# Kernel tuning notes

Measured on AMD Instinct MI355X. Metric: run time of the kernel, lower is better.

Reference implementation:

```python
import jax, jax.numpy as jnp
import numpy as np

SIGMA2 = 1.9 * 1.9   # LJ sigma^2 (Angstrom^2)
EPS = 0.2            # LJ well depth
R2_SOFT = 0.25       # softening to keep energies finite for random dofs


def _local_ht(dofs):
    """dofs [..., 9] -> local homogeneous transform [..., 4, 4].
    Uses (phi, theta, d) bond-style dofs: R = Rz(phi) @ Ry(theta),
    translation d along the rotated x-axis."""
    phi, theta = dofs[..., 0], dofs[..., 1]
    d = 1.5 + 0.25 * jnp.tanh(dofs[..., 2])  # bond length ~1.25..1.75 A
    cp, sp = jnp.cos(phi), jnp.sin(phi)
    ct, st = jnp.cos(theta), jnp.sin(theta)
    r00, r01, r02 = cp * ct, -sp, cp * st
    r10, r11, r12 = sp * ct, cp, sp * st
    r20, r21, r22 = -st, jnp.zeros_like(ct), ct
    tx, ty, tz = d * r00, d * r10, d * r20
    zero, one = jnp.zeros_like(phi), jnp.ones_like(phi)
    ht = jnp.stack([
        jnp.stack([r00, r01, r02, tx], -1),
        jnp.stack([r10, r11, r12, ty], -1),
        jnp.stack([r20, r21, r22, tz], -1),
        jnp.stack([zero, zero, zero, one], -1),
    ], -2)
    return ht


def _forward_kin(full_dofs, P, A):
    # per-pose chain kinforest: cumulative left-product of local HTs
    ht = _local_ht(full_dofs.reshape(P, A, 9))  # [P, A, 4, 4]
    compose = lambda a, b: jnp.einsum('...ij,...jk->...ik', a, b)
    cum = jax.lax.associative_scan(compose, ht, axis=1)
    return cum[..., :3, 3].reshape(-1, 3)  # [P*A, 3]


def _lj_score(coords):
    # coords [P, A, 3] -> per-pose softened LJ energy [P]
    sq = jnp.sum(coords * coords, axis=-1)                 # [P, A]
    G = jnp.einsum('pad,pbd->pab', coords, coords)         # [P, A, A] GEMM
    r2 = sq[:, :, None] + sq[:, None, :] - 2.0 * G + R2_SOFT
    inv6 = (SIGMA2 / r2) ** 3
    e = 4.0 * EPS * (inv6 * inv6 - inv6)
    A = coords.shape[1]
    mask = jnp.triu(jnp.ones((A, A), dtype=coords.dtype), k=1)  # i < j
    return jnp.sum(e * mask, axis=(1, 2))


def setup_inputs() -> dict:
    key = jax.random.key(0)
    k1, k2 = jax.random.split(key)
    P, A = 4, 4096
    full_dofs = 0.5 * jax.random.normal(k1, (P * A, 9), dtype=jnp.float32)
    pose_stack_coords = 5.0 * jax.random.normal(k2, (P, A, 3), dtype=jnp.float32)
    kinforest_id = jnp.arange(P * A, dtype=jnp.int64)
    return {"full_dofs": full_dofs, "pose_stack_coords": pose_stack_coords,
            "kinforest_id": kinforest_id}


def reference(full_dofs, pose_stack_coords, kinforest_id):
    P, A, _ = pose_stack_coords.shape
    kincoords = _forward_kin(full_dofs, P, A)  # [P*A, 3]
    coords = pose_stack_coords.reshape(-1, 3).at[kinforest_id].set(kincoords)
    coords = coords.reshape(P, A, 3)
    return _lj_score(coords)  # [P]
```

## Files before the change

kernel.cpp:

```cpp
#include <hip/hip_runtime.h>
#include <math.h>

#define A_ATOMS 4096
#define P_POSES 4
#define N_TOT   (A_ATOMS * P_POSES)
#define TILE    128
#define NTILES  (A_ATOMS / TILE)
#define NPAIRT  (NTILES * (NTILES + 1) / 2)

#define SEG     64
#define NSEG    (A_ATOMS / SEG)
#define APPLY_T 256
#define APPLY_B (A_ATOMS / APPLY_T)

typedef float v2f __attribute__((ext_vector_type(2)));

__device__ __constant__ float c_SIGMA2  = 1.9f * 1.9f;
__device__ __constant__ float c_4EPS    = 0.8f;
__device__ __constant__ float c_R2SOFT  = 0.25f;

struct RT { float m[12]; };

__device__ inline RT rt_identity() {
    RT v;
    v.m[0]=1.f; v.m[1]=0.f; v.m[2]=0.f;  v.m[3]=0.f;
    v.m[4]=0.f; v.m[5]=1.f; v.m[6]=0.f;  v.m[7]=0.f;
    v.m[8]=0.f; v.m[9]=0.f; v.m[10]=1.f; v.m[11]=0.f;
    return v;
}

__device__ inline RT rt_compose(const RT& a, const RT& b) {
    RT c;
#pragma unroll
    for (int i = 0; i < 3; ++i) {
        float a0 = a.m[i*4+0], a1 = a.m[i*4+1], a2 = a.m[i*4+2];
        c.m[i*4+0] = fmaf(a0, b.m[0], fmaf(a1, b.m[4],  a2*b.m[8]));
        c.m[i*4+1] = fmaf(a0, b.m[1], fmaf(a1, b.m[5],  a2*b.m[9]));
        c.m[i*4+2] = fmaf(a0, b.m[2], fmaf(a1, b.m[6],  a2*b.m[10]));
        c.m[i*4+3] = fmaf(a0, b.m[3], fmaf(a1, b.m[7],  fmaf(a2, b.m[11], a.m[i*4+3])));
    }
    return c;
}

__device__ inline RT rt_shfl_up(const RT& a, int off) {
    RT r;
#pragma unroll
    for (int i = 0; i < 12; ++i) r.m[i] = __shfl_up(a.m[i], off, 64);
    return r;
}

__device__ inline RT local_ht(const float* __restrict__ dof) {
    float phi = dof[0], th = dof[1];
    float d = fmaf(0.25f, tanhf(dof[2]), 1.5f);
    float sp, cp, st, ct;
    sincosf(phi, &sp, &cp);
    sincosf(th,  &st, &ct);
    RT h;
    h.m[0] = cp*ct; h.m[1] = -sp; h.m[2]  = cp*st; h.m[3]  = d*cp*ct;
    h.m[4] = sp*ct; h.m[5] =  cp; h.m[6]  = sp*st; h.m[7]  = d*sp*ct;
    h.m[8] = -st;   h.m[9] = 0.f; h.m[10] = ct;    h.m[11] = -d*st;
    return h;
}

__global__ __launch_bounds__(SEG) void fk_scan(const float* __restrict__ dofs,
                                               float* __restrict__ Tx,
                                               float* __restrict__ Ty,
                                               float* __restrict__ Tz,
                                               float4* __restrict__ S0,
                                               float4* __restrict__ S1,
                                               float4* __restrict__ S2) {
    const int pose = blockIdx.x >> 6;
    const int seg  = blockIdx.x & (NSEG - 1);
    const int lane = threadIdx.x;
    const int g    = pose * A_ATOMS + seg * SEG + lane;

    RT v = local_ht(dofs + (size_t)g * 9);

#pragma unroll
    for (int off = 1; off < 64; off <<= 1) {
        RT l = rt_shfl_up(v, off);
        if (lane >= off) v = rt_compose(l, v);
    }

    Tx[g] = v.m[3]; Ty[g] = v.m[7]; Tz[g] = v.m[11];

    if (lane == 63) {
        int s = pose * NSEG + seg;
        S0[s] = make_float4(v.m[0], v.m[1], v.m[2],  v.m[3]);
        S1[s] = make_float4(v.m[4], v.m[5], v.m[6],  v.m[7]);
        S2[s] = make_float4(v.m[8], v.m[9], v.m[10], v.m[11]);
    }
}

__global__ __launch_bounds__(APPLY_T) void fk_apply(const int* __restrict__ kid,
                                                    const float* __restrict__ Tx,
                                                    const float* __restrict__ Ty,
                                                    const float* __restrict__ Tz,
                                                    const float4* __restrict__ S0,
                                                    const float4* __restrict__ S1,
                                                    const float4* __restrict__ S2,
                                                    float* __restrict__ X,
                                                    float* __restrict__ Y,
                                                    float* __restrict__ Z,
                                                    float* __restrict__ out) {
    __shared__ float4 e0[NSEG], e1[NSEG], e2[NSEG];

    const int pose = blockIdx.y;
    const int blk  = blockIdx.x;
    const int tid  = threadIdx.x;
    if (blk == 0 && tid == 0) out[pose] = 0.f;

    if (tid < 64) {
        int s = pose * NSEG + tid;
        float4 a0 = S0[s], a1 = S1[s], a2 = S2[s];
        RT v;
        v.m[0]=a0.x; v.m[1]=a0.y; v.m[2]=a0.z;  v.m[3]=a0.w;
        v.m[4]=a1.x; v.m[5]=a1.y; v.m[6]=a1.z;  v.m[7]=a1.w;
        v.m[8]=a2.x; v.m[9]=a2.y; v.m[10]=a2.z; v.m[11]=a2.w;
#pragma unroll
        for (int off = 1; off < 64; off <<= 1) {
            RT l = rt_shfl_up(v, off);
            if (tid >= off) v = rt_compose(l, v);
        }
        RT ex = rt_shfl_up(v, 1);
        if (tid == 0) ex = rt_identity();
        e0[tid] = make_float4(ex.m[0], ex.m[1], ex.m[2],  ex.m[3]);
        e1[tid] = make_float4(ex.m[4], ex.m[5], ex.m[6],  ex.m[7]);
        e2[tid] = make_float4(ex.m[8], ex.m[9], ex.m[10], ex.m[11]);
    }
    __syncthreads();

    const int a = blk * APPLY_T + tid;
    const int g = pose * A_ATOMS + a;
    float rx = Tx[g], ry = Ty[g], rz = Tz[g];
    float4 x0 = e0[a >> 6], x1 = e1[a >> 6], x2 = e2[a >> 6];
    float tx = fmaf(x0.x, rx, fmaf(x0.y, ry, fmaf(x0.z, rz, x0.w)));
    float ty = fmaf(x1.x, rx, fmaf(x1.y, ry, fmaf(x1.z, rz, x1.w)));
    float tz = fmaf(x2.x, rx, fmaf(x2.y, ry, fmaf(x2.z, rz, x2.w)));
    int dst = kid[g];
    X[dst] = tx; Y[dst] = ty; Z[dst] = tz;
}

__global__ __launch_bounds__(256) void lj_kernel(const float* __restrict__ X,
                                                 const float* __restrict__ Y,
                                                 const float* __restrict__ Z,
                                                 float* __restrict__ out) {
    const int pose = blockIdx.y;
    int rr = blockIdx.x, bi = 0;
    while (rr >= NTILES - bi) { rr -= NTILES - bi; ++bi; }
    const int bj = bi + rr;

    __shared__ float sxi[TILE], syi[TILE], szi[TILE];
    __shared__ float sxj[TILE], syj[TILE], szj[TILE];

    const int tid = threadIdx.x;
    const float* Xp = X + pose * A_ATOMS;
    const float* Yp = Y + pose * A_ATOMS;
    const float* Zp = Z + pose * A_ATOMS;

    if (tid < TILE) {
        int gi = bi * TILE + tid;
        sxi[tid] = Xp[gi]; syi[tid] = Yp[gi]; szi[tid] = Zp[gi];
    } else {
        int t = tid - TILE;
        int gj = bj * TILE + t;
        sxj[t] = Xp[gj]; syj[t] = Yp[gj]; szj[t] = Zp[gj];
    }
    __syncthreads();

    const int i0 = (tid & 15) * 8;
    const int j0 = (tid >> 4) * 8;

    const float SIG2 = c_SIGMA2, SOFT = c_R2SOFT;
    float acc = 0.f;

    if (bi != bj) {
        float xi[8], yi[8], zi[8];
#pragma unroll
        for (int k = 0; k < 8; ++k) {
            xi[k] = sxi[i0 + k]; yi[k] = syi[i0 + k]; zi[k] = szi[i0 + k];
        }
        v2f xj2[4], yj2[4], zj2[4];
#pragma unroll
        for (int p = 0; p < 4; ++p) {
            xj2[p] = (v2f){sxj[j0 + 2*p], sxj[j0 + 2*p + 1]};
            yj2[p] = (v2f){syj[j0 + 2*p], syj[j0 + 2*p + 1]};
            zj2[p] = (v2f){szj[j0 + 2*p], szj[j0 + 2*p + 1]};
        }
        const v2f soft2 = (v2f){SOFT, SOFT};
        v2f acc2 = (v2f){0.f, 0.f};
#pragma unroll
        for (int p = 0; p < 4; ++p) {
#pragma unroll
            for (int k = 0; k < 8; ++k) {
                v2f dx = xi[k] - xj2[p];
                v2f dy = yi[k] - yj2[p];
                v2f dz = zi[k] - zj2[p];
                v2f r2 = __builtin_elementwise_fma(dx, dx,
                         __builtin_elementwise_fma(dy, dy,
                         __builtin_elementwise_fma(dz, dz, soft2)));
                v2f rc = (v2f){__builtin_amdgcn_rcpf(r2.x), __builtin_amdgcn_rcpf(r2.y)};
                v2f t  = SIG2 * rc;
                v2f i6 = t * t * t;
                acc2 += __builtin_elementwise_fma(i6, i6, -i6);
            }
        }
        acc = acc2.x + acc2.y;
    } else {
        float xi[8], yi[8], zi[8], xj[8], yj[8], zj[8];
#pragma unroll
        for (int k = 0; k < 8; ++k) {
            xi[k] = sxi[i0 + k]; yi[k] = syi[i0 + k]; zi[k] = szi[i0 + k];
            xj[k] = sxj[j0 + k]; yj[k] = syj[j0 + k]; zj[k] = szj[j0 + k];
        }
#pragma unroll
        for (int jj = 0; jj < 8; ++jj) {
            int j = j0 + jj;
#pragma unroll
            for (int k = 0; k < 8; ++k) {
                float dx = xi[k] - xj[jj], dy = yi[k] - yj[jj], dz = zi[k] - zj[jj];
                float r2 = fmaf(dx, dx, fmaf(dy, dy, fmaf(dz, dz, SOFT)));
                float t  = SIG2 * __builtin_amdgcn_rcpf(r2);
                float i6 = t * t * t;
                float hh = fmaf(i6, i6, -i6);
                acc += ((i0 + k) < j) ? hh : 0.f;
            }
        }
    }
    acc *= c_4EPS;

#pragma unroll
    for (int off = 32; off > 0; off >>= 1) acc += __shfl_down(acc, off, 64);

    __shared__ float wsum[4];
    int lane = tid & 63, wid = tid >> 6;
    if (lane == 0) wsum[wid] = acc;
    __syncthreads();
    if (tid == 0) {
        float s = wsum[0] + wsum[1] + wsum[2] + wsum[3];
        atomicAdd(out + pose, s);
    }
}

extern "C" void kernel_launch(void* const* d_in, const int* in_sizes, int n_in,
                              void* d_out, int out_size, void* d_ws, size_t ws_size,
                              hipStream_t stream) {
    (void)in_sizes; (void)n_in; (void)out_size; (void)ws_size;
    const float* dofs = (const float*)d_in[0];
    const int*   kid  = (const int*)d_in[2];
    float*       out  = (float*)d_out;

    float* X  = (float*)d_ws;
    float* Y  = X + N_TOT;
    float* Z  = Y + N_TOT;
    float* Tx = Z + N_TOT;
    float* Ty = Tx + N_TOT;
    float* Tz = Ty + N_TOT;
    float4* S0 = (float4*)(Tz + N_TOT);
    float4* S1 = S0 + P_POSES * NSEG;
    float4* S2 = S1 + P_POSES * NSEG;

    fk_scan<<<P_POSES * NSEG, SEG, 0, stream>>>(dofs, Tx, Ty, Tz, S0, S1, S2);
    dim3 agrid(APPLY_B, P_POSES);
    fk_apply<<<agrid, APPLY_T, 0, stream>>>(kid, Tx, Ty, Tz, S0, S1, S2, X, Y, Z, out);
    dim3 grid(NPAIRT, P_POSES);
    lj_kernel<<<grid, 256, 0, stream>>>(X, Y, Z, out);
}
```

Baseline: 90.91 us.

## Fold segment-prefix apply into LJ tile load, shrink fk_apply to tiny prefix kernel

Result: slower. 93.25 us (+2.6%).

```diff
diff --git a/kernel.cpp b/kernel.cpp
--- a/kernel.cpp
+++ b/kernel.cpp
@@ -10,8 +10,7 @@
 
 #define SEG     64
 #define NSEG    (A_ATOMS / SEG)
-#define APPLY_T 256
-#define APPLY_B (A_ATOMS / APPLY_T)
+#define NSEG_TOT (P_POSES * NSEG)
 
 typedef float v2f __attribute__((ext_vector_type(2)));
 
@@ -63,9 +62,8 @@
 }
 
 __global__ __launch_bounds__(SEG) void fk_scan(const float* __restrict__ dofs,
-                                               float* __restrict__ Tx,
-                                               float* __restrict__ Ty,
-                                               float* __restrict__ Tz,
+                                               const int* __restrict__ kid,
+                                               float4* __restrict__ TS,
                                                float4* __restrict__ S0,
                                                float4* __restrict__ S1,
                                                float4* __restrict__ S2) {
@@ -82,68 +80,49 @@
         if (lane >= off) v = rt_compose(l, v);
     }
 
-    Tx[g] = v.m[3]; Ty[g] = v.m[7]; Tz[g] = v.m[11];
+    const int wseg = pose * NSEG + seg;
+    TS[kid[g]] = make_float4(v.m[3], v.m[7], v.m[11], __int_as_float(wseg));
 
     if (lane == 63) {
-        int s = pose * NSEG + seg;
-        S0[s] = make_float4(v.m[0], v.m[1], v.m[2],  v.m[3]);
-        S1[s] = make_float4(v.m[4], v.m[5], v.m[6],  v.m[7]);
-        S2[s] = make_float4(v.m[8], v.m[9], v.m[10], v.m[11]);
-    }
-}
-
-__global__ __launch_bounds__(APPLY_T) void fk_apply(const int* __restrict__ kid,
-                                                    const float* __restrict__ Tx,
-                                                    const float* __restrict__ Ty,
-                                                    const float* __restrict__ Tz,
-                                                    const float4* __restrict__ S0,
-                                                    const float4* __restrict__ S1,
-                                                    const float4* __restrict__ S2,
-                                                    float* __restrict__ X,
-                                                    float* __restrict__ Y,
-                                                    float* __restrict__ Z,
-                                                    float* __restrict__ out) {
-    __shared__ float4 e0[NSEG], e1[NSEG], e2[NSEG];
-
-    const int pose = blockIdx.y;
-    const int blk  = blockIdx.x;
-    const int tid  = threadIdx.x;
-    if (blk == 0 && tid == 0) out[pose] = 0.f;
-
-    if (tid < 64) {
-        int s = pose * NSEG + tid;
-        float4 a0 = S0[s], a1 = S1[s], a2 = S2[s];
-        RT v;
-        v.m[0]=a0.x; v.m[1]=a0.y; v.m[2]=a0.z;  v.m[3]=a0.w;
-        v.m[4]=a1.x; v.m[5]=a1.y; v.m[6]=a1.z;  v.m[7]=a1.w;
-        v.m[8]=a2.x; v.m[9]=a2.y; v.m[10]=a2.z; v.m[11]=a2.w;
-#pragma unroll
-        for (int off = 1; off < 64; off <<= 1) {
-            RT l = rt_shfl_up(v, off);
-            if (tid >= off) v = rt_compose(l, v);
-        }
-        RT ex = rt_shfl_up(v, 1);
-        if (tid == 0) ex = rt_identity();
-        e0[tid] = make_float4(ex.m[0], ex.m[1], ex.m[2],  ex.m[3]);
-        e1[tid] = make_float4(ex.m[4], ex.m[5], ex.m[6],  ex.m[7]);
-        e2[tid] = make_float4(ex.m[8], ex.m[9], ex.m[10], ex.m[11]);
-    }
-    __syncthreads();
-
-    const int a = blk * APPLY_T + tid;
-    const int g = pose * A_ATOMS + a;
-    float rx = Tx[g], ry = Ty[g], rz = Tz[g];
-    float4 x0 = e0[a >> 6], x1 = e1[a >> 6], x2 = e2[a >> 6];
-    float tx = fmaf(x0.x, rx, fmaf(x0.y, ry, fmaf(x0.z, rz, x0.w)));
-    float ty = fmaf(x1.x, rx, fmaf(x1.y, ry, fmaf(x1.z, rz, x1.w)));
-    float tz = fmaf(x2.x, rx, fmaf(x2.y, ry, fmaf(x2.z, rz, x2.w)));
-    int dst = kid[g];
-    X[dst] = tx; Y[dst] = ty; Z[dst] = tz;
-}
-
-__global__ __launch_bounds__(256) void lj_kernel(const float* __restrict__ X,
-                                                 const float* __restrict__ Y,
-                                                 const float* __restrict__ Z,
+        S0[wseg] = make_float4(v.m[0], v.m[1], v.m[2],  v.m[3]);
+        S1[wseg] = make_float4(v.m[4], v.m[5], v.m[6],  v.m[7]);
+        S2[wseg] = make_float4(v.m[8], v.m[9], v.m[10], v.m[11]);
+    }
+}
+
+__global__ __launch_bounds__(SEG) void fk_eprefix(const float4* __restrict__ S0,
+                                                  const float4* __restrict__ S1,
+                                                  const float4* __restrict__ S2,
+                                                  float4* __restrict__ E0,
+                                                  float4* __restrict__ E1,
+                                                  float4* __restrict__ E2,
+                                                  float* __restrict__ out) {
+    const int pose = blockIdx.x;
+    const int lane = threadIdx.x;
+    if (lane == 0) out[pose] = 0.f;
+
+    const int s = pose * NSEG + lane;
+    float4 a0 = S0[s], a1 = S1[s], a2 = S2[s];
+    RT v;
+    v.m[0]=a0.x; v.m[1]=a0.y; v.m[2]=a0.z;  v.m[3]=a0.w;
+    v.m[4]=a1.x; v.m[5]=a1.y; v.m[6]=a1.z;  v.m[7]=a1.w;
+    v.m[8]=a2.x; v.m[9]=a2.y; v.m[10]=a2.z; v.m[11]=a2.w;
+#pragma unroll
+    for (int off = 1; off < 64; off <<= 1) {
+        RT l = rt_shfl_up(v, off);
+        if (lane >= off) v = rt_compose(l, v);
+    }
+    RT ex = rt_shfl_up(v, 1);
+    if (lane == 0) ex = rt_identity();
+    E0[s] = make_float4(ex.m[0], ex.m[1], ex.m[2],  ex.m[3]);
+    E1[s] = make_float4(ex.m[4], ex.m[5], ex.m[6],  ex.m[7]);
+    E2[s] = make_float4(ex.m[8], ex.m[9], ex.m[10], ex.m[11]);
+}
+
+__global__ __launch_bounds__(256) void lj_kernel(const float4* __restrict__ TS,
+                                                 const float4* __restrict__ E0,
+                                                 const float4* __restrict__ E1,
+                                                 const float4* __restrict__ E2,
                                                  float* __restrict__ out) {
     const int pose = blockIdx.y;
     int rr = blockIdx.x, bi = 0;
@@ -154,17 +133,16 @@
     __shared__ float sxj[TILE], syj[TILE], szj[TILE];
 
     const int tid = threadIdx.x;
-    const float* Xp = X + pose * A_ATOMS;
-    const float* Yp = Y + pose * A_ATOMS;
-    const float* Zp = Z + pose * A_ATOMS;
-
-    if (tid < TILE) {
-        int gi = bi * TILE + tid;
-        sxi[tid] = Xp[gi]; syi[tid] = Yp[gi]; szi[tid] = Zp[gi];
-    } else {
-        int t = tid - TILE;
-        int gj = bj * TILE + t;
-        sxj[t] = Xp[gj]; syj[t] = Yp[gj]; szj[t] = Zp[gj];
+    {
+        const int a_loc = (tid < TILE) ? (bi * TILE + tid) : (bj * TILE + (tid - TILE));
+        float4 t4 = TS[pose * A_ATOMS + a_loc];
+        const int wseg = __float_as_int(t4.w);
+        float4 x0 = E0[wseg], x1 = E1[wseg], x2 = E2[wseg];
+        float x = fmaf(x0.x, t4.x, fmaf(x0.y, t4.y, fmaf(x0.z, t4.z, x0.w)));
+        float y = fmaf(x1.x, t4.x, fmaf(x1.y, t4.y, fmaf(x1.z, t4.z, x1.w)));
+        float z = fmaf(x2.x, t4.x, fmaf(x2.y, t4.y, fmaf(x2.z, t4.z, x2.w)));
+        if (tid < TILE) { sxi[tid] = x; syi[tid] = y; szi[tid] = z; }
+        else            { sxj[tid - TILE] = x; syj[tid - TILE] = y; szj[tid - TILE] = z; }
     }
     __syncthreads();
 
@@ -250,19 +228,16 @@
     const int*   kid  = (const int*)d_in[2];
     float*       out  = (float*)d_out;
 
-    float* X  = (float*)d_ws;
-    float* Y  = X + N_TOT;
-    float* Z  = Y + N_TOT;
-    float* Tx = Z + N_TOT;
-    float* Ty = Tx + N_TOT;
-    float* Tz = Ty + N_TOT;
-    float4* S0 = (float4*)(Tz + N_TOT);
-    float4* S1 = S0 + P_POSES * NSEG;
-    float4* S2 = S1 + P_POSES * NSEG;
-
-    fk_scan<<<P_POSES * NSEG, SEG, 0, stream>>>(dofs, Tx, Ty, Tz, S0, S1, S2);
-    dim3 agrid(APPLY_B, P_POSES);
-    fk_apply<<<agrid, APPLY_T, 0, stream>>>(kid, Tx, Ty, Tz, S0, S1, S2, X, Y, Z, out);
+    float4* TS = (float4*)d_ws;
+    float4* S0 = TS + N_TOT;
+    float4* S1 = S0 + NSEG_TOT;
+    float4* S2 = S1 + NSEG_TOT;
+    float4* E0 = S2 + NSEG_TOT;
+    float4* E1 = E0 + NSEG_TOT;
+    float4* E2 = E1 + NSEG_TOT;
+
+    fk_scan<<<NSEG_TOT, SEG, 0, stream>>>(dofs, kid, TS, S0, S1, S2);
+    fk_eprefix<<<P_POSES, SEG, 0, stream>>>(S0, S1, S2, E0, E1, E2, out);
     dim3 grid(NPAIRT, P_POSES);
-    lj_kernel<<<grid, 256, 0, stream>>>(X, Y, Z, out);
-}
+    lj_kernel<<<grid, 256, 0, stream>>>(TS, E0, E1, E2, out);
+}
```

## Process strips of four j-tiles per block with register-prefetched next tile

Applied to the files above, without the earlier changes.

Result: faster. 76.84 us (-15.5%).

```diff
diff --git a/kernel.cpp b/kernel.cpp
--- a/kernel.cpp
+++ b/kernel.cpp
@@ -6,7 +6,9 @@
 #define N_TOT   (A_ATOMS * P_POSES)
 #define TILE    128
 #define NTILES  (A_ATOMS / TILE)
-#define NPAIRT  (NTILES * (NTILES + 1) / 2)
+#define JG      4
+#define NJG     (NTILES / JG)
+#define NSTRIPS 144
 
 #define SEG     64
 #define NSEG    (A_ATOMS / SEG)
@@ -147,8 +149,9 @@
                                                  float* __restrict__ out) {
     const int pose = blockIdx.y;
     int rr = blockIdx.x, bi = 0;
-    while (rr >= NTILES - bi) { rr -= NTILES - bi; ++bi; }
-    const int bj = bi + rr;
+    while (rr >= NJG - (bi >> 2)) { rr -= NJG - (bi >> 2); ++bi; }
+    const int jg = (bi >> 2) + rr;
+    const int t0 = (jg == (bi >> 2)) ? (bi & 3) : 0;
 
     __shared__ float sxi[TILE], syi[TILE], szi[TILE];
     __shared__ float sxj[TILE], syj[TILE], szj[TILE];
@@ -163,7 +166,7 @@
         sxi[tid] = Xp[gi]; syi[tid] = Yp[gi]; szi[tid] = Zp[gi];
     } else {
         int t = tid - TILE;
-        int gj = bj * TILE + t;
+        int gj = (jg * JG + t0) * TILE + t;
         sxj[t] = Xp[gj]; syj[t] = Yp[gj]; szj[t] = Zp[gj];
     }
     __syncthreads();
@@ -172,59 +175,79 @@
     const int j0 = (tid >> 4) * 8;
 
     const float SIG2 = c_SIGMA2, SOFT = c_R2SOFT;
+
+    float xi[8], yi[8], zi[8];
+#pragma unroll
+    for (int k = 0; k < 8; ++k) {
+        xi[k] = sxi[i0 + k]; yi[k] = syi[i0 + k]; zi[k] = szi[i0 + k];
+    }
+
     float acc = 0.f;
 
-    if (bi != bj) {
-        float xi[8], yi[8], zi[8];
-#pragma unroll
-        for (int k = 0; k < 8; ++k) {
-            xi[k] = sxi[i0 + k]; yi[k] = syi[i0 + k]; zi[k] = szi[i0 + k];
-        }
-        v2f xj2[4], yj2[4], zj2[4];
-#pragma unroll
-        for (int p = 0; p < 4; ++p) {
-            xj2[p] = (v2f){sxj[j0 + 2*p], sxj[j0 + 2*p + 1]};
-            yj2[p] = (v2f){syj[j0 + 2*p], syj[j0 + 2*p + 1]};
-            zj2[p] = (v2f){szj[j0 + 2*p], szj[j0 + 2*p + 1]};
-        }
-        const v2f soft2 = (v2f){SOFT, SOFT};
-        v2f acc2 = (v2f){0.f, 0.f};
-#pragma unroll
-        for (int p = 0; p < 4; ++p) {
+    for (int t = t0; t < JG; ++t) {
+        const int bj = jg * JG + t;
+
+        float px, py, pz;
+        if (t < JG - 1 && tid >= TILE) {
+            int gj = (bj + 1) * TILE + (tid - TILE);
+            px = Xp[gj]; py = Yp[gj]; pz = Zp[gj];
+        }
+
+        if (bi != bj) {
+            v2f xj2[4], yj2[4], zj2[4];
+#pragma unroll
+            for (int p = 0; p < 4; ++p) {
+                xj2[p] = (v2f){sxj[j0 + 2*p], sxj[j0 + 2*p + 1]};
+                yj2[p] = (v2f){syj[j0 + 2*p], syj[j0 + 2*p + 1]};
+                zj2[p] = (v2f){szj[j0 + 2*p], szj[j0 + 2*p + 1]};
+            }
+            const v2f soft2 = (v2f){SOFT, SOFT};
+            v2f acc2 = (v2f){0.f, 0.f};
+#pragma unroll
+            for (int p = 0; p < 4; ++p) {
+#pragma unroll
+                for (int k = 0; k < 8; ++k) {
+                    v2f dx = xi[k] - xj2[p];
+                    v2f dy = yi[k] - yj2[p];
+                    v2f dz = zi[k] - zj2[p];
+                    v2f r2 = __builtin_elementwise_fma(dx, dx,
+                             __builtin_elementwise_fma(dy, dy,
+                             __builtin_elementwise_fma(dz, dz, soft2)));
+                    v2f rc = (v2f){__builtin_amdgcn_rcpf(r2.x), __builtin_amdgcn_rcpf(r2.y)};
+                    v2f tt = SIG2 * rc;
+                    v2f i6 = tt * tt * tt;
+                    acc2 += __builtin_elementwise_fma(i6, i6, -i6);
+                }
+            }
+            acc += acc2.x + acc2.y;
+        } else {
+            float xj[8], yj[8], zj[8];
 #pragma unroll
             for (int k = 0; k < 8; ++k) {
-                v2f dx = xi[k] - xj2[p];
-                v2f dy = yi[k] - yj2[p];
-                v2f dz = zi[k] - zj2[p];
-                v2f r2 = __builtin_elementwise_fma(dx, dx,
-                         __builtin_elementwise_fma(dy, dy,
-                         __builtin_elementwise_fma(dz, dz, soft2)));
-                v2f rc = (v2f){__builtin_amdgcn_rcpf(r2.x), __builtin_amdgcn_rcpf(r2.y)};
-                v2f t  = SIG2 * rc;
-                v2f i6 = t * t * t;
-                acc2 += __builtin_elementwise_fma(i6, i6, -i6);
-            }
-        }
-        acc = acc2.x + acc2.y;
-    } else {
-        float xi[8], yi[8], zi[8], xj[8], yj[8], zj[8];
-#pragma unroll
-        for (int k = 0; k < 8; ++k) {
-            xi[k] = sxi[i0 + k]; yi[k] = syi[i0 + k]; zi[k] = szi[i0 + k];
-            xj[k] = sxj[j0 + k]; yj[k] = syj[j0 + k]; zj[k] = szj[j0 + k];
-        }
-#pragma unroll
-        for (int jj = 0; jj < 8; ++jj) {
-            int j = j0 + jj;
-#pragma unroll
-            for (int k = 0; k < 8; ++k) {
-                float dx = xi[k] - xj[jj], dy = yi[k] - yj[jj], dz = zi[k] - zj[jj];
-                float r2 = fmaf(dx, dx, fmaf(dy, dy, fmaf(dz, dz, SOFT)));
-                float t  = SIG2 * __builtin_amdgcn_rcpf(r2);
-                float i6 = t * t * t;
-                float hh = fmaf(i6, i6, -i6);
-                acc += ((i0 + k) < j) ? hh : 0.f;
-            }
+                xj[k] = sxj[j0 + k]; yj[k] = syj[j0 + k]; zj[k] = szj[j0 + k];
+            }
+#pragma unroll
+            for (int jj = 0; jj < 8; ++jj) {
+                int j = j0 + jj;
+#pragma unroll
+                for (int k = 0; k < 8; ++k) {
+                    float dx = xi[k] - xj[jj], dy = yi[k] - yj[jj], dz = zi[k] - zj[jj];
+                    float r2 = fmaf(dx, dx, fmaf(dy, dy, fmaf(dz, dz, SOFT)));
+                    float tt = SIG2 * __builtin_amdgcn_rcpf(r2);
+                    float i6 = tt * tt * tt;
+                    float hh = fmaf(i6, i6, -i6);
+                    acc += ((i0 + k) < j) ? hh : 0.f;
+                }
+            }
+        }
+
+        if (t < JG - 1) {
+            __syncthreads();
+            if (tid >= TILE) {
+                int tl = tid - TILE;
+                sxj[tl] = px; syj[tl] = py; szj[tl] = pz;
+            }
+            __syncthreads();
         }
     }
     acc *= c_4EPS;
@@ -263,6 +286,6 @@
     fk_scan<<<P_POSES * NSEG, SEG, 0, stream>>>(dofs, Tx, Ty, Tz, S0, S1, S2);
     dim3 agrid(APPLY_B, P_POSES);
     fk_apply<<<agrid, APPLY_T, 0, stream>>>(kid, Tx, Ty, Tz, S0, S1, S2, X, Y, Z, out);
-    dim3 grid(NPAIRT, P_POSES);
+    dim3 grid(NSTRIPS, P_POSES);
     lj_kernel<<<grid, 256, 0, stream>>>(X, Y, Z, out);
 }
```
